# Kernel optimization log

Measured on AMD Instinct MI355X. Metric: run time of the kernel, lower is better.

## Reference

```python
import jax, jax.numpy as jnp
import numpy as np

NUM_HEADS = 8
POS_DIM = 4
LEFT_CTX = 512


def setup_inputs() -> dict:
    key = jax.random.key(0)
    ks = jax.random.split(key, 9)
    S, B, E, A, H, P, L = 512, 16, 512, 512, NUM_HEADS, POS_DIM, LEFT_CTX
    in_out = 2 * A + A // 2 + H * P  # 1312
    S2 = 2 * S - 1 + L  # 1535
    return {
        "x": jax.random.normal(ks[0], (S, B, E), jnp.float32) * 0.1,
        "cached_key": jax.random.normal(ks[1], (L, B, A), jnp.float32) * 0.1,
        "cached_val": jax.random.normal(ks[2], (L, B, A // 2), jnp.float32) * 0.1,
        "pos_emb": jax.random.normal(ks[3], (1, S2, E), jnp.float32) * 0.1,
        "in_proj_w": jax.random.normal(ks[4], (in_out, E), jnp.float32) * 0.02,
        "in_proj_b": jnp.zeros((in_out,), jnp.float32),
        "linear_pos_w": jax.random.normal(ks[5], (H * P, E), jnp.float32) * 0.02,
        "out_proj_w": jax.random.normal(ks[6], (E, A // 2), jnp.float32) * 0.02,
        "out_proj_b": jnp.zeros((E,), jnp.float32),
    }


def reference(x, cached_key, cached_val, pos_emb, in_proj_w, in_proj_b,
              linear_pos_w, out_proj_w, out_proj_b):
    S, B, E = x.shape
    L = cached_key.shape[0]
    A = cached_key.shape[-1]          # attention_dim
    H, P = NUM_HEADS, POS_DIM
    hd = A // H                        # head_dim
    vd = hd // 2                       # value head dim

    # in_proj (nn.Linear): (S, B, 2A + A/2 + H*P)
    xp = jnp.einsum('sbe,oe->sbo', x, in_proj_w) + in_proj_b
    q = xp[..., :A]
    k_new = xp[..., A:2 * A]
    v_new = xp[..., 2 * A:2 * A + A // 2]
    p = xp[..., 2 * A + A // 2:]

    # pad+add == concat(cached, new) along time
    k = jnp.concatenate([cached_key, k_new], axis=0)   # (kv, B, A)
    v = jnp.concatenate([cached_val, v_new], axis=0)   # (kv, B, A/2)
    cached_key_out = k[-L:]
    cached_val_out = v[-L:]
    kv = k.shape[0]

    q4 = q.reshape(S, B, H, hd)
    p4 = p.reshape(S, B, H, P)
    k4 = k.reshape(kv, B, H, hd)
    v4 = v.reshape(kv, B, H, vd)

    # relative position bias: linear_pos has no bias
    S2 = pos_emb.shape[1]              # 2S - 1 + L
    pos = (jnp.einsum('one,pe->onp', pos_emb, linear_pos_w)
           .reshape(S2, H, P))          # (S2, H, P)
    pos_weights = jnp.einsum('sbhp,nhp->bhsn', p4, pos)  # (B, H, S, S2)

    # as_strided relative shift: out[b,h,t,j] = pw[b,h,t, (S-1) - t + j]
    idx = (S - 1) - jnp.arange(S)[:, None] + jnp.arange(kv)[None, :]  # (S, kv)
    pos_weights = jnp.take_along_axis(pos_weights, idx[None, None], axis=3)

    scores = jnp.einsum('sbhd,nbhd->bhsn', q4, k4) + pos_weights  # (B,H,S,kv)
    attn = jax.nn.softmax(scores, axis=-1)

    out = jnp.einsum('bhsn,nbhd->sbhd', attn, v4).reshape(S, B, A // 2)
    out = jnp.einsum('sbd,ed->sbe', out, out_proj_w) + out_proj_b

    weights = attn.reshape(B * H, S, kv)
    return out, weights, cached_key_out, cached_val_out
```

## Files before the change

kernel.cpp:

```cpp
#include <hip/hip_runtime.h>
#include <math.h>


using f32x4  = __attribute__((ext_vector_type(4))) float;
using bf16x8 = __attribute__((ext_vector_type(8))) short;

__device__ __forceinline__ unsigned short f2bf(float f) {
    unsigned u = __builtin_bit_cast(unsigned, f);
    u = (u + 0x7FFFu + ((u >> 16) & 1u)) >> 16;
    return (unsigned short)u;
}
__device__ __forceinline__ float bf2f(unsigned short s) {
    return __builtin_bit_cast(float, (unsigned)s << 16);
}

__device__ __forceinline__ size_t kbf_addr(int bh, int n, int d) {
    return ((((size_t)bh * 64 + (n >> 4)) * 2 + (d >> 5)) * 64
            + ((d & 31) >> 3) * 16 + (n & 15)) * 8 + (d & 7);
}

__device__ __forceinline__ void cvt8(const float* __restrict__ src,
                                     unsigned short* __restrict__ dst, int i)
{
    float4 v0 = *(const float4*)(src + i);
    float4 v1 = *(const float4*)(src + i + 4);
    unsigned short tmp[8] = { f2bf(v0.x), f2bf(v0.y), f2bf(v0.z), f2bf(v0.w),
                              f2bf(v1.x), f2bf(v1.y), f2bf(v1.z), f2bf(v1.w) };
    *(int4*)(dst + i) = *(const int4*)tmp;
}

__global__ __launch_bounds__(256)
void prep(const float* __restrict__ x, const float* __restrict__ in_proj_w,
          const float* __restrict__ out_proj_w, const float* __restrict__ ck_in,
          const float* __restrict__ pos_emb, const float* __restrict__ lpw,
          unsigned short* __restrict__ xb, unsigned short* __restrict__ wb,
          unsigned short* __restrict__ opw, unsigned short* __restrict__ kb,
          float* __restrict__ pos_ws)
{
    __shared__ float As[16][68];
    __shared__ float Bs[16][68];
    const int bid = blockIdx.x, t = threadIdx.x;
    if (bid < 2048) {
        cvt8(x, xb, (bid * 256 + t) * 8);
    } else if (bid < 2376) {
        cvt8(in_proj_w, wb, ((bid - 2048) * 256 + t) * 8);
    } else if (bid < 2440) {
        cvt8(out_proj_w, opw, ((bid - 2376) * 256 + t) * 8);
    } else if (bid < 3464) {
        const int i  = bid - 2440;
        const int n0 = (i & 63) * 8;
        const int b  = i >> 6;
        const int c  = t * 2;
        const int h  = c >> 6, d = c & 63;
        const int bh = b * 8 + h;
        #pragma unroll
        for (int j = 0; j < 8; ++j) {
            const int n = n0 + j;
            float2 v = *(const float2*)(ck_in + ((size_t)n * 16 + b) * 512 + c);
            unsigned short tmp[2] = { f2bf(v.x), f2bf(v.y) };
            *(unsigned int*)(kb + kbf_addr(bh, n, d)) = *(const unsigned int*)tmp;
        }
    } else {
        const int m0 = (bid - 3464) * 64;
        const int lr = t >> 2, lc = (t & 3) * 4;
        const int tx = t & 15, ty = t >> 4;
        float acc[4][4] = {};
        for (int k0 = 0; k0 < 512; k0 += 16) {
            float4 av = make_float4(0.f,0.f,0.f,0.f);
            float4 bv = make_float4(0.f,0.f,0.f,0.f);
            if (m0 + lr < 1535) av = *(const float4*)(pos_emb + (size_t)(m0 + lr) * 512 + k0 + lc);
            if (lr < 32)        bv = *(const float4*)(lpw + (size_t)lr * 512 + k0 + lc);
            __syncthreads();
            As[lc+0][lr] = av.x; As[lc+1][lr] = av.y; As[lc+2][lr] = av.z; As[lc+3][lr] = av.w;
            Bs[lc+0][lr] = bv.x; Bs[lc+1][lr] = bv.y; Bs[lc+2][lr] = bv.z; Bs[lc+3][lr] = bv.w;
            __syncthreads();
            #pragma unroll
            for (int kk = 0; kk < 16; ++kk) {
                float4 a4 = *(const float4*)&As[kk][ty * 4];
                float4 b4 = *(const float4*)&Bs[kk][tx * 4];
                float af[4] = {a4.x, a4.y, a4.z, a4.w};
                float bf[4] = {b4.x, b4.y, b4.z, b4.w};
                #pragma unroll
                for (int i2 = 0; i2 < 4; ++i2)
                    #pragma unroll
                    for (int j = 0; j < 4; ++j)
                        acc[i2][j] += af[i2] * bf[j];
            }
        }
        const int n = tx * 4;
        if (n < 32) {
            #pragma unroll
            for (int i2 = 0; i2 < 4; ++i2) {
                const int mi = m0 + ty * 4 + i2;
                if (mi >= 1535) break;
                #pragma unroll
                for (int j = 0; j < 4; ++j)
                    pos_ws[(size_t)mi * 32 + n + j] = acc[i2][j];
            }
        }
    }
}

__global__ __launch_bounds__(256)
void mfma_gemm_nt(const unsigned short* __restrict__ A,
                  const unsigned short* __restrict__ B,
                  const float* __restrict__ bias, int K, int N, int NBLK, int mode,
                  float* __restrict__ C, int ldc,
                  unsigned short* __restrict__ qb, float* __restrict__ ck,
                  unsigned short* __restrict__ kb, float* __restrict__ cv,
                  float* __restrict__ p_ws)
{
    __shared__ unsigned short smem[6144];
    const int t  = threadIdx.x;
    const int wv = t >> 6, l = t & 63;
    const int lr = l & 15, g = l >> 4;
    const int bid = blockIdx.x;
    const int xcd = bid & 7, i = bid >> 3;
    const int my  = xcd + 8 * (i / NBLK);
    const int nx  = i % NBLK;
    const int m0b = my * 128;
    const int m0  = m0b + wv * 32;
    const int n0  = nx * 64;

    const int srow = t >> 2, soct = t & 3;
    const unsigned short* Ag0 = A + (size_t)(m0b + srow) * K + soct * 8;
    const unsigned short* Ag1 = Ag0 + (size_t)64 * K;
    const unsigned short* Bg  = B + (size_t)(n0 + srow) * K + soct * 8;
    const int oa0 = (soct * 128 + srow) * 8;
    const int oa1 = oa0 + 64 * 8;
    const int ob  = 4096 + (soct * 64 + srow) * 8;

    const int ra0 = (g * 128 + wv * 32 + lr) * 8;
    const int ra1 = ra0 + 16 * 8;
    const int rb  = 4096 + (g * 64 + lr) * 8;

    f32x4 acc[2][4] = {};

    bf16x8 sa0 = *(const bf16x8*)(Ag0);
    bf16x8 sa1 = *(const bf16x8*)(Ag1);
    bf16x8 sb  = *(const bf16x8*)(Bg);

    const int NK = K >> 5;
    for (int t16 = 0; t16 < NK; ++t16) {
        __syncthreads();
        *(bf16x8*)(smem + oa0) = sa0;
        *(bf16x8*)(smem + oa1) = sa1;
        *(bf16x8*)(smem + ob)  = sb;
        __syncthreads();
        if (t16 + 1 < NK) {
            const int k0 = (t16 + 1) * 32;
            sa0 = *(const bf16x8*)(Ag0 + k0);
            sa1 = *(const bf16x8*)(Ag1 + k0);
            sb  = *(const bf16x8*)(Bg + k0);
        }
        bf16x8 a0 = *(const bf16x8*)(smem + ra0);
        bf16x8 a1 = *(const bf16x8*)(smem + ra1);
        bf16x8 b0 = *(const bf16x8*)(smem + rb);
        bf16x8 b1 = *(const bf16x8*)(smem + rb + 16 * 8);
        bf16x8 b2 = *(const bf16x8*)(smem + rb + 32 * 8);
        bf16x8 b3 = *(const bf16x8*)(smem + rb + 48 * 8);
        acc[0][0] = __builtin_amdgcn_mfma_f32_16x16x32_bf16(a0, b0, acc[0][0], 0, 0, 0);
        acc[0][1] = __builtin_amdgcn_mfma_f32_16x16x32_bf16(a0, b1, acc[0][1], 0, 0, 0);
        acc[0][2] = __builtin_amdgcn_mfma_f32_16x16x32_bf16(a0, b2, acc[0][2], 0, 0, 0);
        acc[0][3] = __builtin_amdgcn_mfma_f32_16x16x32_bf16(a0, b3, acc[0][3], 0, 0, 0);
        acc[1][0] = __builtin_amdgcn_mfma_f32_16x16x32_bf16(a1, b0, acc[1][0], 0, 0, 0);
        acc[1][1] = __builtin_amdgcn_mfma_f32_16x16x32_bf16(a1, b1, acc[1][1], 0, 0, 0);
        acc[1][2] = __builtin_amdgcn_mfma_f32_16x16x32_bf16(a1, b2, acc[1][2], 0, 0, 0);
        acc[1][3] = __builtin_amdgcn_mfma_f32_16x16x32_bf16(a1, b3, acc[1][3], 0, 0, 0);
    }

    const int rbase = g * 4;
    const int nf = (N - n0) >= 64 ? 4 : (N - n0) >> 4;
    #pragma unroll
    for (int fi = 0; fi < 2; ++fi) {
        #pragma unroll
        for (int fj = 0; fj < 4; ++fj) {
            if (fj < nf) {
                const f32x4& a = acc[fi][fj];
                const int c = n0 + fj * 16 + lr;
                const float bs = bias ? bias[c] : 0.f;
                #pragma unroll
                for (int r = 0; r < 4; ++r) {
                    const int m = m0 + fi * 16 + rbase + r;
                    const float v = a[r] + bs;
                    if (mode == 0) {
                        C[(size_t)m * ldc + c] = v;
                    } else {
                        const int s = m >> 4, bb = m & 15;
                        if (c < 512) {
                            const int hh = c >> 6, dd = c & 63;
                            qb[(((size_t)bb*8 + hh)*512 + s)*64 + dd] = f2bf(v);
                        } else if (c < 1024) {
                            const int cc = c - 512;
                            __builtin_nontemporal_store(v, ck + (size_t)m * 512 + cc);
                            const int hh = cc >> 6, dd = cc & 63;
                            kb[kbf_addr(bb * 8 + hh, 512 + s, dd)] = f2bf(v);
                        } else if (c < 1280) {
                            cv[(size_t)m * 256 + (c - 1024)] = v;
                        } else {
                            p_ws[(size_t)m * 32 + (c - 1280)] = v;
                        }
                    }
                }
            }
        }
    }
}

__global__ __launch_bounds__(256)
void transpose_v(const float* __restrict__ cv_in, const float* __restrict__ cv_new,
                 unsigned short* __restrict__ vtf)
{
    const int t  = threadIdx.x;
    const int n0 = blockIdx.x * 128;
    const int bh = blockIdx.y;
    const int b  = bh >> 3, h = bh & 7;

    __shared__ float tile[128][33];

    #pragma unroll
    for (int k = 0; k < 4; ++k) {
        const int nl = (t >> 3) + k * 32;
        const int n  = n0 + nl;
        const int c4 = (t & 7) * 4;
        const float* src = (n < 512)
            ? cv_in  + ((size_t)n * 16 + b) * 256 + h * 32 + c4
            : cv_new + ((size_t)(n - 512) * 16 + b) * 256 + h * 32 + c4;
        float4 v = *(const float4*)src;
        tile[nl][c4 + 0] = v.x; tile[nl][c4 + 1] = v.y;
        tile[nl][c4 + 2] = v.z; tile[nl][c4 + 3] = v.w;
    }
    __syncthreads();
    {
        const int l = t & 63, kidxl = t >> 6;
        const int lr = l & 15, ks = (l >> 4) * 8;
        const int kidx = (n0 >> 5) + kidxl;
        #pragma unroll
        for (int dt = 0; dt < 2; ++dt) {
            unsigned short tmp[8];
            #pragma unroll
            for (int j = 0; j < 8; ++j)
                tmp[j] = f2bf(tile[kidxl * 32 + ks + j][dt * 16 + lr]);
            *(int4*)(vtf + ((((size_t)bh * 32 + kidx) * 2 + dt) * 64 + l) * 8)
                = *(const int4*)tmp;
        }
    }
}

__global__ __launch_bounds__(256, 4)
void attn_fused2(const unsigned short* __restrict__ qb,
                 const float* __restrict__ p_ws,
                 const float* __restrict__ pos_ws,
                 const unsigned short* __restrict__ kbf,
                 const unsigned short* __restrict__ vtf,
                 float* __restrict__ weights,
                 unsigned short* __restrict__ ao)
{
    const int t  = threadIdx.x;
    const int wv = t >> 6, l = t & 63;
    const int lr = l & 15, ks0 = (l >> 4) * 8, rbase = (l >> 4) * 4;
    const int idx = blockIdx.x;
    const int kq  = idx >> 3;
    const int bh  = (idx & 7) + 8 * (kq >> 5);
    const int s0  = (kq & 31) * 16;
    const int b   = bh >> 3, h = bh & 7;

    union SM { float4 pos[1039]; unsigned short e[16][1064]; };
    __shared__ SM u;
    __shared__ float pvred[4][16][16];
    __shared__ float red_l[4][16];

    const int j0 = 496 - s0;
    for (int j = t; j < 1039; j += 256)
        u.pos[j] = *(const float4*)(pos_ws + (size_t)(j0 + j) * 32 + h * 4);

    const unsigned short* qp = qb + ((size_t)bh * 512 + s0 + lr) * 64 + ks0;
    bf16x8 qa0 = *(const bf16x8*)(qp);
    bf16x8 qa1 = *(const bf16x8*)(qp + 32);

    float4 p4r[4];
    #pragma unroll
    for (int r = 0; r < 4; ++r)
        p4r[r] = *(const float4*)(p_ws + ((size_t)(s0 + rbase + r) * 16 + b) * 32 + h * 4);

    const unsigned short* kbase = kbf
        + (((size_t)bh * 64 + wv * 16) * 2) * 512 + (size_t)l * 8;
    f32x4 sc[16];
    #pragma unroll
    for (int i = 0; i < 16; ++i) sc[i] = (f32x4){0.f,0.f,0.f,0.f};

    #pragma unroll
    for (int tile = 0; tile < 16; ++tile) {
        bf16x8 k0 = *(const bf16x8*)(kbase + tile * 1024);
        bf16x8 k1 = *(const bf16x8*)(kbase + tile * 1024 + 512);
        sc[tile] = __builtin_amdgcn_mfma_f32_16x16x32_bf16(qa0, k0, sc[tile], 0, 0, 0);
        sc[tile] = __builtin_amdgcn_mfma_f32_16x16x32_bf16(qa1, k1, sc[tile], 0, 0, 0);
    }

    __syncthreads();

    float sm[4] = {0.f, 0.f, 0.f, 0.f};
    #pragma unroll
    for (int tile = 0; tile < 16; ++tile) {
        const int nidx = wv * 256 + tile * 16 + lr;
        #pragma unroll
        for (int r = 0; r < 4; ++r) {
            float4 pp = u.pos[15 - rbase - r + nidx];
            float e = __expf(sc[tile][r] + p4r[r].x * pp.x + p4r[r].y * pp.y
                                         + p4r[r].z * pp.z + p4r[r].w * pp.w);
            sc[tile][r] = e;
            sm[r] += e;
        }
    }
    #pragma unroll
    for (int r = 0; r < 4; ++r) {
        #pragma unroll
        for (int off = 1; off < 16; off <<= 1) sm[r] += __shfl_xor(sm[r], off);
    }

    __syncthreads();

    if (lr == 0) {
        #pragma unroll
        for (int r = 0; r < 4; ++r) red_l[wv][rbase + r] = sm[r];
    }
    #pragma unroll
    for (int tile = 0; tile < 16; ++tile) {
        const int nidx = wv * 256 + tile * 16 + lr;
        #pragma unroll
        for (int r = 0; r < 4; ++r)
            u.e[rbase + r][nidx] = f2bf(sc[tile][r]);
    }
    __syncthreads();

    const int kh = wv >> 1, dt = wv & 1;
    f32x4 paA = {0.f, 0.f, 0.f, 0.f}, paB = {0.f, 0.f, 0.f, 0.f};
    const unsigned short* vbase = vtf
        + (((size_t)bh * 32 + kh * 16) * 2 + dt) * 512 + (size_t)l * 8;
    #pragma unroll
    for (int kstep = 0; kstep < 8; ++kstep) {
        const int kk = kh * 512 + kstep * 32 + ks0;
        bf16x8 wa = *(const bf16x8*)&u.e[lr][kk];
        bf16x8 vb = *(const bf16x8*)(vbase + kstep * 1024);
        paA = __builtin_amdgcn_mfma_f32_16x16x32_bf16(wa, vb, paA, 0, 0, 0);
    }
    #pragma unroll
    for (int kstep = 8; kstep < 16; ++kstep) {
        const int kk = kh * 512 + kstep * 32 + ks0;
        bf16x8 wa = *(const bf16x8*)&u.e[lr][kk];
        bf16x8 vb = *(const bf16x8*)(vbase + kstep * 1024);
        paB = __builtin_amdgcn_mfma_f32_16x16x32_bf16(wa, vb, paB, 0, 0, 0);
    }

    const size_t wb_base = ((size_t)bh * 512 + s0) * 1024;
    #pragma unroll
    for (int i2 = 0; i2 < 8; ++i2) {
        const int id2 = t + i2 * 256;
        const int r   = id2 >> 7;
        const int c8  = (id2 & 127) * 8;
        const float il = 1.0f / (red_l[0][r] + red_l[1][r] + red_l[2][r] + red_l[3][r]);
        bf16x8 ev = *(const bf16x8*)&u.e[r][c8];
        f32x4 o0, o1;
        o0[0] = bf2f((unsigned short)ev[0]) * il;
        o0[1] = bf2f((unsigned short)ev[1]) * il;
        o0[2] = bf2f((unsigned short)ev[2]) * il;
        o0[3] = bf2f((unsigned short)ev[3]) * il;
        o1[0] = bf2f((unsigned short)ev[4]) * il;
        o1[1] = bf2f((unsigned short)ev[5]) * il;
        o1[2] = bf2f((unsigned short)ev[6]) * il;
        o1[3] = bf2f((unsigned short)ev[7]) * il;
        __builtin_nontemporal_store(o0, (f32x4*)(weights + wb_base + (size_t)r * 1024 + c8));
        __builtin_nontemporal_store(o1, (f32x4*)(weights + wb_base + (size_t)r * 1024 + c8 + 4));
    }

    #pragma unroll
    for (int r = 0; r < 4; ++r)
        pvred[wv][rbase + r][lr] = paA[r] + paB[r];
    __syncthreads();
    #pragma unroll
    for (int i3 = 0; i3 < 2; ++i3) {
        const int id3 = t + i3 * 256;
        const int r = id3 >> 5, d = id3 & 31;
        const int dt2 = d >> 4, dl = d & 15;
        const float il = 1.0f / (red_l[0][r] + red_l[1][r] + red_l[2][r] + red_l[3][r]);
        float v = (pvred[dt2][r][dl] + pvred[2 + dt2][r][dl]) * il;
        ao[((size_t)(s0 + r) * 16 + b) * 256 + h * 32 + d] = f2bf(v);
    }
}

extern "C" void kernel_launch(void* const* d_in, const int* in_sizes, int n_in,
                              void* d_out, int out_size, void* d_ws, size_t ws_size,
                              hipStream_t stream)
{
    const float* x            = (const float*)d_in[0];
    const float* cached_key   = (const float*)d_in[1];
    const float* cached_val   = (const float*)d_in[2];
    const float* pos_emb      = (const float*)d_in[3];
    const float* in_proj_w    = (const float*)d_in[4];
    const float* in_proj_b    = (const float*)d_in[5];
    const float* linear_pos_w = (const float*)d_in[6];
    const float* out_proj_w   = (const float*)d_in[7];
    const float* out_proj_b   = (const float*)d_in[8];

    float* out     = (float*)d_out;
    float* weights = out + 4194304;
    float* ck_new  = weights + 67108864;
    float* cv_new  = ck_new + 4194304;

    float* ws      = (float*)d_ws;
    float* p_ws    = ws;
    float* pos_ws  = ws + 262144;
    unsigned short* ao_b  = (unsigned short*)(ws + 311264);
    unsigned short* opw_b = (unsigned short*)(ws + 1359840);
    unsigned short* qb    = (unsigned short*)(ws + 1425376);
    unsigned short* kbf   = (unsigned short*)(ws + 3522528);
    unsigned short* vtf   = (unsigned short*)(ws + 7716832);
    unsigned short* xb    = (unsigned short*)(ws + 9813984);
    unsigned short* wb    = (unsigned short*)(ws + 11911136);

    prep<<<3488, 256, 0, stream>>>(x, in_proj_w, out_proj_w, cached_key,
                                   pos_emb, linear_pos_w,
                                   xb, wb, opw_b, kbf, pos_ws);
    mfma_gemm_nt<<<1344, 256, 0, stream>>>(xb, wb, in_proj_b, 512, 1312, 21, 1,
                                           nullptr, 0,
                                           qb, ck_new, kbf, cv_new, p_ws);
    transpose_v<<<dim3(8, 128), 256, 0, stream>>>(cached_val, cv_new, vtf);
    attn_fused2<<<4096, 256, 0, stream>>>(qb, p_ws, pos_ws, kbf, vtf,
                                          weights, ao_b);
    mfma_gemm_nt<<<512, 256, 0, stream>>>(ao_b, opw_b, out_proj_b, 256, 512, 8, 0,
                                          out, 512,
                                          nullptr, nullptr, nullptr, nullptr,
                                          nullptr);
}
```

Baseline: 182.8 us.

## Process 32 query rows per attention block with 512 threads

Each attention block now handles 32 query rows with 8 wavefronts instead of 16 rows with 4, halving the grid. Each block loads the relative-position table once for twice as many rows, which cuts redundant pos loads and per-block overhead. The PV stage and its reduction are remapped so wave pairs split over key halves, row halves and value-dim halves. LDS use per block roughly doubles (about 68KB), which may lower how many blocks fit per CU and reduce occupancy.

New measurement: 218.4 us. 1.19x slower.

```diff
diff --git a/kernel.cpp b/kernel.cpp
--- a/kernel.cpp
+++ b/kernel.cpp
@@ -247,8 +247,8 @@
     }
 }
 
-__global__ __launch_bounds__(256, 4)
-void attn_fused2(const unsigned short* __restrict__ qb,
+__global__ __launch_bounds__(512, 4)
+void attn_fused3(const unsigned short* __restrict__ qb,
                  const float* __restrict__ p_ws,
                  const float* __restrict__ pos_ws,
                  const unsigned short* __restrict__ kbf,
@@ -261,30 +261,33 @@
     const int lr = l & 15, ks0 = (l >> 4) * 8, rbase = (l >> 4) * 4;
     const int idx = blockIdx.x;
     const int kq  = idx >> 3;
-    const int bh  = (idx & 7) + 8 * (kq >> 5);
-    const int s0  = (kq & 31) * 16;
+    const int bh  = (idx & 7) + 8 * (kq >> 4);
+    const int s0  = (kq & 15) * 32;
     const int b   = bh >> 3, h = bh & 7;
 
-    union SM { float4 pos[1039]; unsigned short e[16][1064]; };
+    union SM { float4 pos[1055]; unsigned short e[32][1064]; };
     __shared__ SM u;
-    __shared__ float pvred[4][16][16];
-    __shared__ float red_l[4][16];
-
-    const int j0 = 496 - s0;
-    for (int j = t; j < 1039; j += 256)
+    __shared__ float pvred[2][32][33];
+    __shared__ float red_l[4][32];
+
+    const int j0 = 480 - s0;
+    for (int j = t; j < 1055; j += 512)
         u.pos[j] = *(const float4*)(pos_ws + (size_t)(j0 + j) * 32 + h * 4);
 
-    const unsigned short* qp = qb + ((size_t)bh * 512 + s0 + lr) * 64 + ks0;
+    const int sh = wv >> 2, nc = wv & 3;
+    const int srow = s0 + sh * 16;
+
+    const unsigned short* qp = qb + ((size_t)bh * 512 + srow + lr) * 64 + ks0;
     bf16x8 qa0 = *(const bf16x8*)(qp);
     bf16x8 qa1 = *(const bf16x8*)(qp + 32);
 
     float4 p4r[4];
     #pragma unroll
     for (int r = 0; r < 4; ++r)
-        p4r[r] = *(const float4*)(p_ws + ((size_t)(s0 + rbase + r) * 16 + b) * 32 + h * 4);
+        p4r[r] = *(const float4*)(p_ws + ((size_t)(srow + rbase + r) * 16 + b) * 32 + h * 4);
 
     const unsigned short* kbase = kbf
-        + (((size_t)bh * 64 + wv * 16) * 2) * 512 + (size_t)l * 8;
+        + (((size_t)bh * 64 + nc * 16) * 2) * 512 + (size_t)l * 8;
     f32x4 sc[16];
     #pragma unroll
     for (int i = 0; i < 16; ++i) sc[i] = (f32x4){0.f,0.f,0.f,0.f};
@@ -302,10 +305,10 @@
     float sm[4] = {0.f, 0.f, 0.f, 0.f};
     #pragma unroll
     for (int tile = 0; tile < 16; ++tile) {
-        const int nidx = wv * 256 + tile * 16 + lr;
+        const int nidx = nc * 256 + tile * 16 + lr;
         #pragma unroll
         for (int r = 0; r < 4; ++r) {
-            float4 pp = u.pos[15 - rbase - r + nidx];
+            float4 pp = u.pos[31 - sh * 16 - rbase - r + nidx];
             float e = __expf(sc[tile][r] + p4r[r].x * pp.x + p4r[r].y * pp.y
                                          + p4r[r].z * pp.z + p4r[r].w * pp.w);
             sc[tile][r] = e;
@@ -322,40 +325,40 @@
 
     if (lr == 0) {
         #pragma unroll
-        for (int r = 0; r < 4; ++r) red_l[wv][rbase + r] = sm[r];
+        for (int r = 0; r < 4; ++r) red_l[nc][sh * 16 + rbase + r] = sm[r];
     }
     #pragma unroll
     for (int tile = 0; tile < 16; ++tile) {
-        const int nidx = wv * 256 + tile * 16 + lr;
+        const int nidx = nc * 256 + tile * 16 + lr;
         #pragma unroll
         for (int r = 0; r < 4; ++r)
-            u.e[rbase + r][nidx] = f2bf(sc[tile][r]);
+            u.e[sh * 16 + rbase + r][nidx] = f2bf(sc[tile][r]);
     }
     __syncthreads();
 
-    const int kh = wv >> 1, dt = wv & 1;
+    const int kh2 = wv >> 2, sh2 = (wv >> 1) & 1, dt = wv & 1;
     f32x4 paA = {0.f, 0.f, 0.f, 0.f}, paB = {0.f, 0.f, 0.f, 0.f};
-    const unsigned short* vbase = vtf
-        + (((size_t)bh * 32 + kh * 16) * 2 + dt) * 512 + (size_t)l * 8;
     #pragma unroll
     for (int kstep = 0; kstep < 8; ++kstep) {
-        const int kk = kh * 512 + kstep * 32 + ks0;
-        bf16x8 wa = *(const bf16x8*)&u.e[lr][kk];
-        bf16x8 vb = *(const bf16x8*)(vbase + kstep * 1024);
+        const int kt = kh2 * 16 + kstep;
+        bf16x8 wa = *(const bf16x8*)&u.e[sh2 * 16 + lr][kt * 32 + ks0];
+        bf16x8 vb = *(const bf16x8*)(vtf
+            + (((size_t)bh * 32 + kt) * 2 + dt) * 512 + (size_t)l * 8);
         paA = __builtin_amdgcn_mfma_f32_16x16x32_bf16(wa, vb, paA, 0, 0, 0);
     }
     #pragma unroll
     for (int kstep = 8; kstep < 16; ++kstep) {
-        const int kk = kh * 512 + kstep * 32 + ks0;
-        bf16x8 wa = *(const bf16x8*)&u.e[lr][kk];
-        bf16x8 vb = *(const bf16x8*)(vbase + kstep * 1024);
+        const int kt = kh2 * 16 + kstep;
+        bf16x8 wa = *(const bf16x8*)&u.e[sh2 * 16 + lr][kt * 32 + ks0];
+        bf16x8 vb = *(const bf16x8*)(vtf
+            + (((size_t)bh * 32 + kt) * 2 + dt) * 512 + (size_t)l * 8);
         paB = __builtin_amdgcn_mfma_f32_16x16x32_bf16(wa, vb, paB, 0, 0, 0);
     }
 
     const size_t wb_base = ((size_t)bh * 512 + s0) * 1024;
     #pragma unroll
     for (int i2 = 0; i2 < 8; ++i2) {
-        const int id2 = t + i2 * 256;
+        const int id2 = t + i2 * 512;
         const int r   = id2 >> 7;
         const int c8  = (id2 & 127) * 8;
         const float il = 1.0f / (red_l[0][r] + red_l[1][r] + red_l[2][r] + red_l[3][r]);
@@ -375,15 +378,14 @@
 
     #pragma unroll
     for (int r = 0; r < 4; ++r)
-        pvred[wv][rbase + r][lr] = paA[r] + paB[r];
+        pvred[kh2][sh2 * 16 + rbase + r][dt * 16 + lr] = paA[r] + paB[r];
     __syncthreads();
     #pragma unroll
     for (int i3 = 0; i3 < 2; ++i3) {
-        const int id3 = t + i3 * 256;
+        const int id3 = t + i3 * 512;
         const int r = id3 >> 5, d = id3 & 31;
-        const int dt2 = d >> 4, dl = d & 15;
         const float il = 1.0f / (red_l[0][r] + red_l[1][r] + red_l[2][r] + red_l[3][r]);
-        float v = (pvred[dt2][r][dl] + pvred[2 + dt2][r][dl]) * il;
+        float v = (pvred[0][r][d] + pvred[1][r][d]) * il;
         ao[((size_t)(s0 + r) * 16 + b) * 256 + h * 32 + d] = f2bf(v);
     }
 }
@@ -425,7 +427,7 @@
                                            nullptr, 0,
                                            qb, ck_new, kbf, cv_new, p_ws);
     transpose_v<<<dim3(8, 128), 256, 0, stream>>>(cached_val, cv_new, vtf);
-    attn_fused2<<<4096, 256, 0, stream>>>(qb, p_ws, pos_ws, kbf, vtf,
+    attn_fused3<<<2048, 512, 0, stream>>>(qb, p_ws, pos_ws, kbf, vtf,
                                           weights, ao_b);
     mfma_gemm_nt<<<512, 256, 0, stream>>>(ao_b, opw_b, out_proj_b, 256, 512, 8, 0,
                                           out, 512,
```
